# Performance work log

Hardware: AMD Instinct MI355X
Metric: run time of the kernel (lower is better)

The kernel has to match this reference:

```python
import jax, jax.numpy as jnp
import numpy as np

B, S = 2, 2048
D_MODEL, N_HEAD = 2048, 16
D_K = D_MODEL // N_HEAD        # 128
D_C, D_CQ = 512, 1024
D_ROPE = 64
D_NOPE = D_K - D_ROPE          # 64
EPS = 1.1920929e-07            # torch.finfo(float32).eps (nn.RMSNorm default)


def rms_norm(x, w):
    var = jnp.mean(x * x, axis=-1, keepdims=True)
    return x * jax.lax.rsqrt(var + EPS) * w


def setup_inputs() -> dict:
    key = jax.random.key(0)
    ks = jax.random.split(key, 16)
    g = lambda k, shape: (jax.random.normal(k, shape, dtype=jnp.float32) * 0.02)
    return {
        "x": jax.random.normal(ks[0], (B, S, D_MODEL), dtype=jnp.float32),
        "q_down_w": g(ks[1], (D_CQ, D_MODEL)),
        "q_down_b": g(ks[2], (D_CQ,)),
        "q_norm_w": jnp.ones((D_CQ,), jnp.float32),
        "q_up_w": g(ks[3], (N_HEAD * D_K, D_CQ)),
        "q_up_b": g(ks[4], (N_HEAD * D_K,)),
        "kv_down_w": g(ks[5], (D_C, D_MODEL)),
        "kv_down_b": g(ks[6], (D_C,)),
        "kv_norm_w": jnp.ones((D_C,), jnp.float32),
        "kv_up_w": g(ks[7], (N_HEAD * (D_NOPE + D_K), D_C)),
        "kv_up_b": g(ks[8], (N_HEAD * (D_NOPE + D_K),)),
        "k_rope_w": g(ks[9], (N_HEAD * D_ROPE, D_MODEL)),
        "k_rope_b": g(ks[10], (N_HEAD * D_ROPE,)),
        "out_w": g(ks[11], (D_MODEL, D_MODEL)),
        "out_b": g(ks[12], (D_MODEL,)),
    }


def reference(x, q_down_w, q_down_b, q_norm_w, q_up_w, q_up_b,
              kv_down_w, kv_down_b, kv_norm_w, kv_up_w, kv_up_b,
              k_rope_w, k_rope_b, out_w, out_b):
    b, s, _ = x.shape
    # Q low-rank path: down -> RMSNorm -> up
    c_q = rms_norm(x @ q_down_w.T + q_down_b, q_norm_w)              # [b,s,d_cq]
    q = (c_q @ q_up_w.T + q_up_b).reshape(b, s, N_HEAD, D_K)
    q = jnp.transpose(q, (0, 2, 1, 3))                               # [b,h,s,d_k]
    q_nope, q_rope = q[..., :D_NOPE], q[..., D_NOPE:]
    # KV low-rank path
    c_kv = rms_norm(x @ kv_down_w.T + kv_down_b, kv_norm_w)          # [b,s,d_c]
    kv = (c_kv @ kv_up_w.T + kv_up_b).reshape(b, s, N_HEAD, D_NOPE + D_K)
    kv = jnp.transpose(kv, (0, 2, 1, 3))                             # [b,h,s,d_nope+d_k]
    k_nope, v = kv[..., :D_NOPE], kv[..., D_NOPE:]
    # decoupled rope subspace (rope=None config: no rotation applied)
    k_rope = (x @ k_rope_w.T + k_rope_b).reshape(b, s, N_HEAD, D_ROPE)
    k_rope = jnp.transpose(k_rope, (0, 2, 1, 3))                     # [b,h,s,d_rope]
    q = jnp.concatenate([q_nope, q_rope], axis=-1)                   # [b,h,s,d_k]
    k = jnp.concatenate([k_nope, k_rope], axis=-1)                   # [b,h,s,d_k]
    # causal attention
    scores = jnp.einsum('bhnd,bhmd->bhnm', q, k) / np.sqrt(D_K).astype(np.float32)
    mask = jnp.tril(jnp.ones((s, s), dtype=bool))
    scores = jnp.where(mask, scores, -jnp.inf)
    probs = jax.nn.softmax(scores, axis=-1)
    attn = jnp.einsum('bhnm,bhmd->bhnd', probs, v)                   # [b,h,s,d_k]
    attn = jnp.transpose(attn, (0, 2, 1, 3)).reshape(b, s, D_MODEL)
    return attn @ out_w.T + out_b
```

## Files before the change

kernel.cpp:

```cpp
#include <hip/hip_runtime.h>
#include <hip/hip_bf16.h>

typedef __attribute__((ext_vector_type(8))) short bf16x8;
typedef __attribute__((ext_vector_type(4))) float f32x4;
typedef __attribute__((ext_vector_type(16))) float f32x16;
typedef unsigned short u16;
typedef unsigned int u32;

#define RMS_EPS 1.1920929e-07f

constexpr int Bb = 2, Ss = 2048, DM = 2048, NH = 16;
constexpr int MROWS = Bb * Ss;

__device__ __forceinline__ u16 f2bf(float f) {
    __hip_bfloat16 h = __float2bfloat16(f);
    return *reinterpret_cast<u16*>(&h);
}

__device__ __forceinline__ float exp2_fast(float x) {
    float r; asm("v_exp_f32 %0, %1" : "=v"(r) : "v"(x)); return r;
}

__device__ __forceinline__ void gload16(const void* g, void* l) {
    __builtin_amdgcn_global_load_lds(
        (const __attribute__((address_space(1))) unsigned int*)g,
        (__attribute__((address_space(3))) unsigned int*)l, 16, 0, 0);
}

__global__ __launch_bounds__(256) void cvt_all(
    const float* __restrict__ s0, u16* __restrict__ d0,
    const float* __restrict__ s1, u16* __restrict__ d1,
    const float* __restrict__ s2, u16* __restrict__ d2,
    const float* __restrict__ s3, u16* __restrict__ d3,
    const float* __restrict__ s4, u16* __restrict__ d4,
    const float* __restrict__ s5, u16* __restrict__ d5,
    const float* __restrict__ s6, u16* __restrict__ d6)
{
    int i = blockIdx.x * 256 + threadIdx.x;
    const float* s; u16* d; int off;
    if (i < 2097152)      { s = s0; d = d0; off = 0; }
    else if (i < 2621440) { s = s1; d = d1; off = 2097152; }
    else if (i < 2883584) { s = s2; d = d2; off = 2621440; }
    else if (i < 3407872) { s = s3; d = d3; off = 2883584; }
    else if (i < 3932160) { s = s4; d = d4; off = 3407872; }
    else if (i < 4325376) { s = s5; d = d5; off = 3932160; }
    else                  { s = s6; d = d6; off = 4325376; }
    int j = i - off;
    float4 v = reinterpret_cast<const float4*>(s)[j];
    ushort4 o;
    o.x = f2bf(v.x); o.y = f2bf(v.y); o.z = f2bf(v.z); o.w = f2bf(v.w);
    reinterpret_cast<ushort4*>(d)[j] = o;
}

__global__ void build_bcat(const float* __restrict__ qb, const float* __restrict__ kvb,
                           const float* __restrict__ krb, float* __restrict__ bcat) {
    int i = blockIdx.x * 256 + threadIdx.x;
    if (i < 1024) bcat[i] = qb[i];
    else if (i < 1536) bcat[i] = kvb[i - 1024];
    else if (i < 2560) bcat[i] = krb[i - 1536];
}

__device__ __forceinline__ void xcd_remap(int& bx, int& by) {
    int nx = gridDim.x, ny = gridDim.y;
    int nwg = nx * ny;
    if ((nwg & 7) != 0) return;
    int flat = blockIdx.x + nx * blockIdx.y;
    int chunk = nwg >> 3;
    int wg = (flat & 7) * chunk + (flat >> 3);
    by = wg % ny;
    bx = wg / ny;
}

template <typename OutT>
__global__ __launch_bounds__(256) void gemm_bt(
    const u16* __restrict__ A, const u16* __restrict__ Bt,
    const float* __restrict__ bias, OutT* __restrict__ C,
    int M, int N, int K)
{
    __shared__ alignas(16) u16 sA[2][128 * 32];
    __shared__ alignas(16) u16 sB[2][128 * 32];
    const int tid = threadIdx.x;
    const int lane = tid & 63;
    const int w = tid >> 6;
    const int wr = w >> 1, wc = w & 1;
    const int l16 = lane & 15, lq = lane >> 4;
    int bx = blockIdx.x, by = blockIdx.y;
    xcd_remap(bx, by);
    const int tileM = by * 128;
    const int tileN = bx * 128;

    f32x4 acc[4][4];
#pragma unroll
    for (int m = 0; m < 4; m++)
#pragma unroll
        for (int n = 0; n < 4; n++)
#pragma unroll
            for (int r = 0; r < 4; r++) acc[m][n][r] = 0.f;

    const int srow = w * 16 + (lane >> 2);
    const int scol = (lane & 3) * 8;
    const u16* gA0 = A + (size_t)(tileM + srow) * K + scol;
    const u16* gA1 = A + (size_t)(tileM + srow + 64) * K + scol;
    const u16* gB0 = Bt + (size_t)(tileN + srow) * K + scol;
    const u16* gB1 = Bt + (size_t)(tileN + srow + 64) * K + scol;
    u16* lA0 = &sA[0][0] + w * 512;
    u16* lA1 = &sA[0][0] + 2048 + w * 512;
    u16* lB0 = &sB[0][0] + w * 512;
    u16* lB1 = &sB[0][0] + 2048 + w * 512;

    int aoff[4], boff[4];
#pragma unroll
    for (int m = 0; m < 4; m++) aoff[m] = (wr * 64 + m * 16 + l16) * 32 + lq * 8;
#pragma unroll
    for (int n = 0; n < 4; n++) boff[n] = (wc * 64 + n * 16 + l16) * 32 + lq * 8;

    const int nk = K >> 5;
    gload16(gA0, lA0);
    gload16(gA1, lA1);
    gload16(gB0, lB0);
    gload16(gB1, lB1);
    __syncthreads();
    int cur = 0;
    for (int kk = 0; kk < nk; ++kk) {
        if (kk + 1 < nk) {
            int nb = (cur ^ 1) * 4096;
            const u16* a0 = gA0 + (size_t)(kk + 1) * 32;
            const u16* a1 = gA1 + (size_t)(kk + 1) * 32;
            const u16* b0 = gB0 + (size_t)(kk + 1) * 32;
            const u16* b1 = gB1 + (size_t)(kk + 1) * 32;
            gload16(a0, lA0 + nb);
            gload16(a1, lA1 + nb);
            gload16(b0, lB0 + nb);
            gload16(b1, lB1 + nb);
        }
        const u16* bA = &sA[0][0] + cur * 4096;
        const u16* bB = &sB[0][0] + cur * 4096;
        bf16x8 af[4], bfr[4];
#pragma unroll
        for (int m = 0; m < 4; m++) af[m] = *(const bf16x8*)&bA[aoff[m]];
#pragma unroll
        for (int n = 0; n < 4; n++) bfr[n] = *(const bf16x8*)&bB[boff[n]];
        __builtin_amdgcn_s_setprio(1);
#pragma unroll
        for (int m = 0; m < 4; m++)
#pragma unroll
            for (int n = 0; n < 4; n++)
                acc[m][n] = __builtin_amdgcn_mfma_f32_16x16x32_bf16(af[m], bfr[n], acc[m][n], 0, 0, 0);
        __builtin_amdgcn_s_setprio(0);
        __syncthreads();
        cur ^= 1;
    }

#pragma unroll
    for (int n = 0; n < 4; n++) {
        int col = tileN + wc * 64 + n * 16 + l16;
        float bv = bias ? bias[col] : 0.f;
#pragma unroll
        for (int m = 0; m < 4; m++) {
            int rowb = tileM + wr * 64 + m * 16 + (lq << 2);
#pragma unroll
            for (int r = 0; r < 4; r++) {
                float v = acc[m][n][r] + bv;
                if constexpr (sizeof(OutT) == 2)
                    C[(size_t)(rowb + r) * N + col] = (OutT)f2bf(v);
                else
                    C[(size_t)(rowb + r) * N + col] = (OutT)v;
            }
        }
    }
}

__global__ __launch_bounds__(256) void gemm_down(
    const u16* __restrict__ A, const u16* __restrict__ Bt,
    const float* __restrict__ bcat, float* __restrict__ dcat,
    u16* __restrict__ krbuf)
{
    constexpr int K = 2048;
    __shared__ alignas(16) u16 sA[2][128 * 32];
    __shared__ alignas(16) u16 sB[2][128 * 32];
    const int tid = threadIdx.x;
    const int lane = tid & 63;
    const int w = tid >> 6;
    const int wr = w >> 1, wc = w & 1;
    const int l16 = lane & 15, lq = lane >> 4;
    int bx = blockIdx.x, by = blockIdx.y;
    xcd_remap(bx, by);
    const int tileM = by * 128;
    const int tileN = bx * 128;

    f32x4 acc[4][4];
#pragma unroll
    for (int m = 0; m < 4; m++)
#pragma unroll
        for (int n = 0; n < 4; n++)
#pragma unroll
            for (int r = 0; r < 4; r++) acc[m][n][r] = 0.f;

    const int srow = w * 16 + (lane >> 2);
    const int scol = (lane & 3) * 8;
    const u16* gA0 = A + (size_t)(tileM + srow) * K + scol;
    const u16* gA1 = A + (size_t)(tileM + srow + 64) * K + scol;
    const u16* gB0 = Bt + (size_t)(tileN + srow) * K + scol;
    const u16* gB1 = Bt + (size_t)(tileN + srow + 64) * K + scol;
    u16* lA0 = &sA[0][0] + w * 512;
    u16* lA1 = &sA[0][0] + 2048 + w * 512;
    u16* lB0 = &sB[0][0] + w * 512;
    u16* lB1 = &sB[0][0] + 2048 + w * 512;

    int aoff[4], boff[4];
#pragma unroll
    for (int m = 0; m < 4; m++) aoff[m] = (wr * 64 + m * 16 + l16) * 32 + lq * 8;
#pragma unroll
    for (int n = 0; n < 4; n++) boff[n] = (wc * 64 + n * 16 + l16) * 32 + lq * 8;

    const int nk = K >> 5;
    gload16(gA0, lA0);
    gload16(gA1, lA1);
    gload16(gB0, lB0);
    gload16(gB1, lB1);
    __syncthreads();
    int cur = 0;
    for (int kk = 0; kk < nk; ++kk) {
        if (kk + 1 < nk) {
            int nb = (cur ^ 1) * 4096;
            const u16* a0 = gA0 + (size_t)(kk + 1) * 32;
            const u16* a1 = gA1 + (size_t)(kk + 1) * 32;
            const u16* b0 = gB0 + (size_t)(kk + 1) * 32;
            const u16* b1 = gB1 + (size_t)(kk + 1) * 32;
            gload16(a0, lA0 + nb);
            gload16(a1, lA1 + nb);
            gload16(b0, lB0 + nb);
            gload16(b1, lB1 + nb);
        }
        const u16* bA = &sA[0][0] + cur * 4096;
        const u16* bB = &sB[0][0] + cur * 4096;
        bf16x8 af[4], bfr[4];
#pragma unroll
        for (int m = 0; m < 4; m++) af[m] = *(const bf16x8*)&bA[aoff[m]];
#pragma unroll
        for (int n = 0; n < 4; n++) bfr[n] = *(const bf16x8*)&bB[boff[n]];
        __builtin_amdgcn_s_setprio(1);
#pragma unroll
        for (int m = 0; m < 4; m++)
#pragma unroll
            for (int n = 0; n < 4; n++)
                acc[m][n] = __builtin_amdgcn_mfma_f32_16x16x32_bf16(af[m], bfr[n], acc[m][n], 0, 0, 0);
        __builtin_amdgcn_s_setprio(0);
        __syncthreads();
        cur ^= 1;
    }

    const bool isrope = (tileN >= 1536);
#pragma unroll
    for (int n = 0; n < 4; n++) {
        int col = tileN + wc * 64 + n * 16 + l16;
        float bv = bcat[col];
#pragma unroll
        for (int m = 0; m < 4; m++) {
            int rowb = tileM + wr * 64 + m * 16 + (lq << 2);
#pragma unroll
            for (int r = 0; r < 4; r++) {
                float v = acc[m][n][r] + bv;
                if (!isrope) dcat[(size_t)(rowb + r) * 1536 + col] = v;
                else         krbuf[(size_t)(rowb + r) * 1024 + (col - 1536)] = f2bf(v);
            }
        }
    }
}

template <int C>
__global__ __launch_bounds__(256) void rmsnorm_bf16(
    const float* __restrict__ in, int istride, const float* __restrict__ wgt, u16* __restrict__ out)
{
    const int row = blockIdx.x;
    const int tid = threadIdx.x;
    constexpr int PER = C / 256;
    const float* p = in + (size_t)row * istride;
    float v[PER];
    float ss = 0.f;
#pragma unroll
    for (int i = 0; i < PER; i++) { v[i] = p[tid + i * 256]; ss += v[i] * v[i]; }
#pragma unroll
    for (int o = 32; o; o >>= 1) ss += __shfl_xor(ss, o, 64);
    __shared__ float red[4];
    if ((tid & 63) == 0) red[tid >> 6] = ss;
    __syncthreads();
    float tot = red[0] + red[1] + red[2] + red[3];
    float inv = rsqrtf(tot / (float)C + RMS_EPS);
    u16* q = out + (size_t)row * C;
#pragma unroll
    for (int i = 0; i < PER; i++) {
        int c = tid + i * 256;
        q[c] = f2bf(v[i] * inv * wgt[c]);
    }
}

__global__ __launch_bounds__(256) void transpose_v(
    const u16* __restrict__ kvbuf, u16* __restrict__ vT)
{
    __shared__ alignas(16) u16 tile[64][72];
    const int tid = threadIdx.x;
    const int t0 = blockIdx.x * 64;
    const int h = blockIdx.y >> 1, dh = blockIdx.y & 1;
    const int trow = tid >> 2, c8 = (tid & 3) * 8;
    const u16* src = kvbuf + (size_t)(t0 + trow) * 3072 + h * 192 + 64 + dh * 64 + c8;
    *(bf16x8*)&tile[trow][c8]      = *(const bf16x8*)src;
    *(bf16x8*)&tile[trow][c8 + 32] = *(const bf16x8*)(src + 32);
    __syncthreads();
    const int drow = tid >> 2, tc8 = (tid & 3) * 8;
    bf16x8 a, b2;
#pragma unroll
    for (int j = 0; j < 8; j++) {
        a[j]  = (short)tile[tc8 + j][drow];
        b2[j] = (short)tile[tc8 + 32 + j][drow];
    }
    u16* dst = vT + (size_t)(h * 128 + dh * 64 + drow) * MROWS + t0 + tc8;
    *(bf16x8*)dst = a;
    *(bf16x8*)(dst + 32) = b2;
}

__global__ __launch_bounds__(256, 2) void mla_attn(
    const u16* __restrict__ qbuf,
    const u16* __restrict__ kvbuf,
    const u16* __restrict__ krbuf,
    const u16* __restrict__ vT,
    u16* __restrict__ obuf)
{
    const int bh = blockIdx.x;
    const int y = blockIdx.y;
    const int ii = y & 7, jj = y >> 3;
    const int qt = jj ? (15 - 2 * ii) : (2 * ii);
    const int b = bh >> 4, hh = bh & 15;
    const int tid = threadIdx.x, lane = tid & 63, w = tid >> 6;
    const int l31 = lane & 31, hx = lane >> 5;

    __shared__ alignas(16) u16 sK[64 * 128];
    __shared__ alignas(16) u16 sVt[128 * 64];

    const int rowbase = b * Ss;
    const int q0 = qt * 128;
    const int nkt = 2 * qt + 2;

    const int sr = tid >> 2, sc = (tid & 3) * 32;
    const int vd = tid >> 1, vh = (tid & 1) * 32;
    const float C1 = 0.12751742f;
    const float THRR = 90.5f;

    bf16x8 qf[8];
    {
        const u16* qp = qbuf + (size_t)(rowbase + q0 + w * 32 + l31) * 2048 + hh * 128;
#pragma unroll
        for (int c = 0; c < 8; c++) qf[c] = *(const bf16x8*)(qp + (2 * c + hx) * 8);
    }
    float mi = -3e38f, li = 0.f;
    f32x16 o[4];
#pragma unroll
    for (int d = 0; d < 4; d++)
#pragma unroll
        for (int i = 0; i < 16; i++) o[d][i] = 0.f;

    bf16x8 kr[4], vr[4];
    {
        const int krow = rowbase + sr;
        const u16* src = (sc < 64)
            ? kvbuf + (size_t)krow * 3072 + hh * 192 + sc
            : krbuf + (size_t)krow * 1024 + hh * 64 + (sc - 64);
#pragma unroll
        for (int j = 0; j < 4; j++) kr[j] = *(const bf16x8*)(src + j * 8);
        const u16* vsrc = vT + (size_t)(hh * 128 + vd) * MROWS + rowbase + vh;
#pragma unroll
        for (int j = 0; j < 4; j++) vr[j] = *(const bf16x8*)(vsrc + j * 8);
    }

#pragma unroll 1
    for (int kt = 0; kt < nkt; ++kt) {
        __syncthreads();
#pragma unroll
        for (int j = 0; j < 4; j++) {
            int byteoff = sr * 256 + (sc + j * 8) * 2;
            *(bf16x8*)((char*)sK + (byteoff ^ ((sr & 7) << 4))) = kr[j];
        }
#pragma unroll
        for (int j = 0; j < 4; j++) {
            int byteoff = vd * 128 + (vh + j * 8) * 2;
            *(bf16x8*)((char*)sVt + (byteoff ^ ((vd & 7) << 4))) = vr[j];
        }
        __syncthreads();
        if (kt + 1 < nkt) {
            const int krow = rowbase + (kt + 1) * 64 + sr;
            const u16* src = (sc < 64)
                ? kvbuf + (size_t)krow * 3072 + hh * 192 + sc
                : krbuf + (size_t)krow * 1024 + hh * 64 + (sc - 64);
#pragma unroll
            for (int j = 0; j < 4; j++) kr[j] = *(const bf16x8*)(src + j * 8);
            const u16* vsrc = vT + (size_t)(hh * 128 + vd) * MROWS + rowbase + (kt + 1) * 64 + vh;
#pragma unroll
            for (int j = 0; j < 4; j++) vr[j] = *(const bf16x8*)(vsrc + j * 8);
        }

        const bool alive = (kt * 64) <= (q0 + w * 32 + 31);
        if (alive) {
            f32x16 scf[2];
#pragma unroll
            for (int b2 = 0; b2 < 2; b2++)
#pragma unroll
                for (int i = 0; i < 16; i++) scf[b2][i] = 0.f;
            __builtin_amdgcn_s_setprio(1);
#pragma unroll
            for (int s = 0; s < 8; s++) {
#pragma unroll
                for (int b2 = 0; b2 < 2; b2++) {
                    int krow = b2 * 32 + l31;
                    int kbyte = (krow * 256 + s * 32 + hx * 16) ^ ((l31 & 7) << 4);
                    bf16x8 kf = *(const bf16x8*)((char*)sK + kbyte);
                    scf[b2] = __builtin_amdgcn_mfma_f32_32x32x16_bf16(kf, qf[s], scf[b2], 0, 0, 0);
                }
            }
            __builtin_amdgcn_s_setprio(0);

            if (kt * 64 + 63 > q0 + w * 32) {
                const int qg = q0 + w * 32 + l31;
#pragma unroll
                for (int b2 = 0; b2 < 2; b2++)
#pragma unroll
                    for (int rg = 0; rg < 16; rg++) {
                        int kg = kt * 64 + b2 * 32 + (rg & 3) + 8 * (rg >> 2) + 4 * hx;
                        if (kg > qg) scf[b2][rg] = -3e38f;
                    }
            }
            float mx = mi;
#pragma unroll
            for (int b2 = 0; b2 < 2; b2++)
#pragma unroll
                for (int rg = 0; rg < 16; rg++) mx = fmaxf(mx, scf[b2][rg]);
            mx = fmaxf(mx, __shfl_xor(mx, 32, 64));
            if (!__all(mx - mi <= THRR)) {
                float f = exp2_fast((mi - mx) * C1);
                li *= f;
#pragma unroll
                for (int d = 0; d < 4; d++)
#pragma unroll
                    for (int i = 0; i < 16; i++) o[d][i] *= f;
                mi = mx;
            }
            float mc = mi * C1;
            float rs = 0.f;
#pragma unroll
            for (int b2 = 0; b2 < 2; b2++)
#pragma unroll
                for (int rg = 0; rg < 16; rg++) {
                    float pv = exp2_fast(__fmaf_rn(scf[b2][rg], C1, -mc));
                    scf[b2][rg] = pv;
                    rs += pv;
                }
            rs += __shfl_xor(rs, 32, 64);
            li += rs;

            u32 pk[2][4][2];
#pragma unroll
            for (int b2 = 0; b2 < 2; b2++)
#pragma unroll
                for (int g = 0; g < 4; g++) {
                    pk[b2][g][0] = (u32)f2bf(scf[b2][4 * g + 0]) | ((u32)f2bf(scf[b2][4 * g + 1]) << 16);
                    pk[b2][g][1] = (u32)f2bf(scf[b2][4 * g + 2]) | ((u32)f2bf(scf[b2][4 * g + 3]) << 16);
                }

            __builtin_amdgcn_s_setprio(1);
#pragma unroll
            for (int t = 0; t < 4; t++) {
                const int b2 = t >> 1, s = t & 1;
                u32 send0 = hx ? pk[b2][2 * s][0] : pk[b2][2 * s + 1][0];
                u32 send1 = hx ? pk[b2][2 * s][1] : pk[b2][2 * s + 1][1];
                u32 r0 = (u32)__shfl_xor((int)send0, 32, 64);
                u32 r1 = (u32)__shfl_xor((int)send1, 32, 64);
                union { u32 wd[4]; bf16x8 v; } pu;
                pu.wd[0] = hx ? r0 : pk[b2][2 * s][0];
                pu.wd[1] = hx ? r1 : pk[b2][2 * s][1];
                pu.wd[2] = hx ? pk[b2][2 * s + 1][0] : r0;
                pu.wd[3] = hx ? pk[b2][2 * s + 1][1] : r1;
#pragma unroll
                for (int dblk = 0; dblk < 4; dblk++) {
                    int vrow = dblk * 32 + l31;
                    int vbyte = (vrow * 128 + t * 32 + hx * 16) ^ ((l31 & 7) << 4);
                    bf16x8 vf = *(const bf16x8*)((char*)sVt + vbyte);
                    o[dblk] = __builtin_amdgcn_mfma_f32_32x32x16_bf16(vf, pu.v, o[dblk], 0, 0, 0);
                }
            }
            __builtin_amdgcn_s_setprio(0);
        }
    }
    float invl = 1.f / li;
    u16* op = obuf + (size_t)(rowbase + q0 + w * 32 + l31) * 2048 + hh * 128;
#pragma unroll
    for (int dblk = 0; dblk < 4; dblk++)
#pragma unroll
        for (int rg = 0; rg < 4; rg++) {
            int d0 = dblk * 32 + rg * 8 + hx * 4;
            ushort4 ov;
            ov.x = f2bf(o[dblk][rg * 4 + 0] * invl);
            ov.y = f2bf(o[dblk][rg * 4 + 1] * invl);
            ov.z = f2bf(o[dblk][rg * 4 + 2] * invl);
            ov.w = f2bf(o[dblk][rg * 4 + 3] * invl);
            *(ushort4*)(op + d0) = ov;
        }
}

extern "C" void kernel_launch(void* const* d_in, const int* in_sizes, int n_in,
                              void* d_out, int out_size, void* d_ws, size_t ws_size,
                              hipStream_t stream) {
    const float* x        = (const float*)d_in[0];
    const float* q_down_w = (const float*)d_in[1];
    const float* q_down_b = (const float*)d_in[2];
    const float* q_norm_w = (const float*)d_in[3];
    const float* q_up_w   = (const float*)d_in[4];
    const float* q_up_b   = (const float*)d_in[5];
    const float* kv_down_w= (const float*)d_in[6];
    const float* kv_down_b= (const float*)d_in[7];
    const float* kv_norm_w= (const float*)d_in[8];
    const float* kv_up_w  = (const float*)d_in[9];
    const float* kv_up_b  = (const float*)d_in[10];
    const float* k_rope_w = (const float*)d_in[11];
    const float* k_rope_b = (const float*)d_in[12];
    const float* out_w    = (const float*)d_in[13];
    const float* out_b    = (const float*)d_in[14];

    char* ws = (char*)d_ws;
    u16* xbf    = (u16*)(ws + 0);
    u16* wcat   = (u16*)(ws + 16777216);
    u16* quw    = (u16*)(ws + 27262976);
    u16* kvuw   = (u16*)(ws + 31457280);
    u16* outw   = (u16*)(ws + 34603008);
    float* bcat = (float*)(ws + 42991616);
    float* dcat = (float*)(ws + 43008000);
    u16* cq     = (u16*)(ws + 68173824);
    u16* ckv    = (u16*)(ws + 76562432);
    u16* qbuf   = (u16*)(ws + 80756736);
    u16* kvbuf  = (u16*)(ws + 97533952);
    u16* krbuf  = (u16*)(ws + 122699776);
    u16* vT     = (u16*)(ws + 0);
    u16* attnbuf= (u16*)(ws + 43008000);

    cvt_all<<<20992, 256, 0, stream>>>(
        x, xbf,
        q_down_w,  wcat,
        kv_down_w, wcat + 1024 * 2048,
        k_rope_w,  wcat + 1536 * 2048,
        q_up_w,    quw,
        kv_up_w,   kvuw,
        out_w,     outw);
    build_bcat<<<10, 256, 0, stream>>>(q_down_b, kv_down_b, k_rope_b, bcat);

    gemm_down<<<dim3(20, 32), 256, 0, stream>>>(xbf, wcat, bcat, dcat, krbuf);
    rmsnorm_bf16<1024><<<MROWS, 256, 0, stream>>>(dcat, 1536, q_norm_w, cq);
    rmsnorm_bf16<512><<<MROWS, 256, 0, stream>>>(dcat + 1024, 1536, kv_norm_w, ckv);
    gemm_bt<u16><<<dim3(16, 32), 256, 0, stream>>>(cq, quw, q_up_b, qbuf, MROWS, 2048, 1024);
    gemm_bt<u16><<<dim3(24, 32), 256, 0, stream>>>(ckv, kvuw, kv_up_b, kvbuf, MROWS, 3072, 512);
    transpose_v<<<dim3(64, 32), 256, 0, stream>>>(kvbuf, vT);
    mla_attn<<<dim3(32, 16), 256, 0, stream>>>(qbuf, kvbuf, krbuf, vT, attnbuf);
    gemm_bt<float><<<dim3(16, 32), 256, 0, stream>>>(attnbuf, outw, out_b, (float*)d_out, MROWS, 2048, 2048);
}
```

Before: 262.3 us.

## Split attention KV range across two wave groups and merge softmax partials

```diff
diff --git a/kernel.cpp b/kernel.cpp
--- a/kernel.cpp
+++ b/kernel.cpp
@@ -319,7 +319,7 @@
     *(bf16x8*)(dst + 32) = b2;
 }
 
-__global__ __launch_bounds__(256, 2) void mla_attn(
+__global__ __launch_bounds__(512, 4) void mla_attn(
     const u16* __restrict__ qbuf,
     const u16* __restrict__ kvbuf,
     const u16* __restrict__ krbuf,
@@ -331,18 +331,26 @@
     const int ii = y & 7, jj = y >> 3;
     const int qt = jj ? (15 - 2 * ii) : (2 * ii);
     const int b = bh >> 4, hh = bh & 15;
-    const int tid = threadIdx.x, lane = tid & 63, w = tid >> 6;
+    const int tid = threadIdx.x, lane = tid & 63;
+    const int w8 = tid >> 6;
+    const int grp = w8 >> 2;
+    const int w = w8 & 3;
     const int l31 = lane & 31, hx = lane >> 5;
-
-    __shared__ alignas(16) u16 sK[64 * 128];
-    __shared__ alignas(16) u16 sVt[128 * 64];
+    const int tg = tid & 255;
+
+    __shared__ alignas(16) char smem[68608];
+    char* sK  = smem + grp * 16384;
+    char* sVt = smem + 32768 + grp * 16384;
+    float* mO  = (float*)smem;
+    float* mml = (float*)(smem + 67584);
 
     const int rowbase = b * Ss;
     const int q0 = qt * 128;
-    const int nkt = 2 * qt + 2;
-
-    const int sr = tid >> 2, sc = (tid & 3) * 32;
-    const int vd = tid >> 1, vh = (tid & 1) * 32;
+    const int niter = qt + 1;
+    const int kbase = grp ? niter : 0;
+
+    const int sr = tg >> 2, sc = (tg & 3) * 32;
+    const int vd = tg >> 1, vh = (tg & 1) * 32;
     const float C1 = 0.12751742f;
     const float THRR = 90.5f;
 
@@ -361,32 +369,33 @@
 
     bf16x8 kr[4], vr[4];
     {
-        const int krow = rowbase + sr;
+        const int krow = rowbase + kbase * 64 + sr;
         const u16* src = (sc < 64)
             ? kvbuf + (size_t)krow * 3072 + hh * 192 + sc
             : krbuf + (size_t)krow * 1024 + hh * 64 + (sc - 64);
 #pragma unroll
         for (int j = 0; j < 4; j++) kr[j] = *(const bf16x8*)(src + j * 8);
-        const u16* vsrc = vT + (size_t)(hh * 128 + vd) * MROWS + rowbase + vh;
+        const u16* vsrc = vT + (size_t)(hh * 128 + vd) * MROWS + rowbase + kbase * 64 + vh;
 #pragma unroll
         for (int j = 0; j < 4; j++) vr[j] = *(const bf16x8*)(vsrc + j * 8);
     }
 
 #pragma unroll 1
-    for (int kt = 0; kt < nkt; ++kt) {
+    for (int t = 0; t < niter; ++t) {
+        const int kt = kbase + t;
         __syncthreads();
 #pragma unroll
         for (int j = 0; j < 4; j++) {
             int byteoff = sr * 256 + (sc + j * 8) * 2;
-            *(bf16x8*)((char*)sK + (byteoff ^ ((sr & 7) << 4))) = kr[j];
+            *(bf16x8*)(sK + (byteoff ^ ((sr & 7) << 4))) = kr[j];
         }
 #pragma unroll
         for (int j = 0; j < 4; j++) {
             int byteoff = vd * 128 + (vh + j * 8) * 2;
-            *(bf16x8*)((char*)sVt + (byteoff ^ ((vd & 7) << 4))) = vr[j];
+            *(bf16x8*)(sVt + (byteoff ^ ((vd & 7) << 4))) = vr[j];
         }
         __syncthreads();
-        if (kt + 1 < nkt) {
+        if (t + 1 < niter) {
             const int krow = rowbase + (kt + 1) * 64 + sr;
             const u16* src = (sc < 64)
                 ? kvbuf + (size_t)krow * 3072 + hh * 192 + sc
@@ -412,7 +421,7 @@
                 for (int b2 = 0; b2 < 2; b2++) {
                     int krow = b2 * 32 + l31;
                     int kbyte = (krow * 256 + s * 32 + hx * 16) ^ ((l31 & 7) << 4);
-                    bf16x8 kf = *(const bf16x8*)((char*)sK + kbyte);
+                    bf16x8 kf = *(const bf16x8*)(sK + kbyte);
                     scf[b2] = __builtin_amdgcn_mfma_f32_32x32x16_bf16(kf, qf[s], scf[b2], 0, 0, 0);
                 }
             }
@@ -467,8 +476,8 @@
 
             __builtin_amdgcn_s_setprio(1);
 #pragma unroll
-            for (int t = 0; t < 4; t++) {
-                const int b2 = t >> 1, s = t & 1;
+            for (int t4 = 0; t4 < 4; t4++) {
+                const int b2 = t4 >> 1, s = t4 & 1;
                 u32 send0 = hx ? pk[b2][2 * s][0] : pk[b2][2 * s + 1][0];
                 u32 send1 = hx ? pk[b2][2 * s][1] : pk[b2][2 * s + 1][1];
                 u32 r0 = (u32)__shfl_xor((int)send0, 32, 64);
@@ -481,28 +490,55 @@
 #pragma unroll
                 for (int dblk = 0; dblk < 4; dblk++) {
                     int vrow = dblk * 32 + l31;
-                    int vbyte = (vrow * 128 + t * 32 + hx * 16) ^ ((l31 & 7) << 4);
-                    bf16x8 vf = *(const bf16x8*)((char*)sVt + vbyte);
+                    int vbyte = (vrow * 128 + t4 * 32 + hx * 16) ^ ((l31 & 7) << 4);
+                    bf16x8 vf = *(const bf16x8*)(sVt + vbyte);
                     o[dblk] = __builtin_amdgcn_mfma_f32_32x32x16_bf16(vf, pu.v, o[dblk], 0, 0, 0);
                 }
             }
             __builtin_amdgcn_s_setprio(0);
         }
     }
-    float invl = 1.f / li;
-    u16* op = obuf + (size_t)(rowbase + q0 + w * 32 + l31) * 2048 + hh * 128;
-#pragma unroll
-    for (int dblk = 0; dblk < 4; dblk++)
-#pragma unroll
-        for (int rg = 0; rg < 4; rg++) {
-            int d0 = dblk * 32 + rg * 8 + hx * 4;
-            ushort4 ov;
-            ov.x = f2bf(o[dblk][rg * 4 + 0] * invl);
-            ov.y = f2bf(o[dblk][rg * 4 + 1] * invl);
-            ov.z = f2bf(o[dblk][rg * 4 + 2] * invl);
-            ov.w = f2bf(o[dblk][rg * 4 + 3] * invl);
-            *(ushort4*)(op + d0) = ov;
-        }
+
+    __syncthreads();
+    if (grp) {
+#pragma unroll
+        for (int dblk = 0; dblk < 4; dblk++)
+#pragma unroll
+            for (int rg = 0; rg < 4; rg++) {
+                int d0 = dblk * 32 + rg * 8 + hx * 4;
+                f32x4 v;
+                v[0] = o[dblk][rg * 4 + 0]; v[1] = o[dblk][rg * 4 + 1];
+                v[2] = o[dblk][rg * 4 + 2]; v[3] = o[dblk][rg * 4 + 3];
+                *(f32x4*)&mO[(w * 32 + l31) * 132 + d0] = v;
+            }
+        if (hx == 0) {
+            mml[(w * 32 + l31) * 2 + 0] = mi;
+            mml[(w * 32 + l31) * 2 + 1] = li;
+        }
+    }
+    __syncthreads();
+    if (!grp) {
+        float mB = mml[(w * 32 + l31) * 2 + 0];
+        float lB = mml[(w * 32 + l31) * 2 + 1];
+        float m = fmaxf(mi, mB);
+        float a0 = exp2_fast((mi - m) * C1);
+        float a1 = exp2_fast((mB - m) * C1);
+        float linv = 1.f / (li * a0 + lB * a1);
+        u16* op = obuf + (size_t)(rowbase + q0 + w * 32 + l31) * 2048 + hh * 128;
+#pragma unroll
+        for (int dblk = 0; dblk < 4; dblk++)
+#pragma unroll
+            for (int rg = 0; rg < 4; rg++) {
+                int d0 = dblk * 32 + rg * 8 + hx * 4;
+                f32x4 ob = *(const f32x4*)&mO[(w * 32 + l31) * 132 + d0];
+                ushort4 ov;
+                ov.x = f2bf((o[dblk][rg * 4 + 0] * a0 + ob[0] * a1) * linv);
+                ov.y = f2bf((o[dblk][rg * 4 + 1] * a0 + ob[1] * a1) * linv);
+                ov.z = f2bf((o[dblk][rg * 4 + 2] * a0 + ob[2] * a1) * linv);
+                ov.w = f2bf((o[dblk][rg * 4 + 3] * a0 + ob[3] * a1) * linv);
+                *(ushort4*)(op + d0) = ov;
+            }
+    }
 }
 
 extern "C" void kernel_launch(void* const* d_in, const int* in_sizes, int n_in,
@@ -556,6 +592,6 @@
     gemm_bt<u16><<<dim3(16, 32), 256, 0, stream>>>(cq, quw, q_up_b, qbuf, MROWS, 2048, 1024);
     gemm_bt<u16><<<dim3(24, 32), 256, 0, stream>>>(ckv, kvuw, kv_up_b, kvbuf, MROWS, 3072, 512);
     transpose_v<<<dim3(64, 32), 256, 0, stream>>>(kvbuf, vT);
-    mla_attn<<<dim3(32, 16), 256, 0, stream>>>(qbuf, kvbuf, krbuf, vT, attnbuf);
+    mla_attn<<<dim3(32, 16), 512, 0, stream>>>(qbuf, kvbuf, krbuf, vT, attnbuf);
     gemm_bt<float><<<dim3(16, 32), 256, 0, stream>>>(attnbuf, outw, out_b, (float*)d_out, MROWS, 2048, 2048);
 }
```

After: 447.3 us. +70.5%, slower.
